# Optimization experiments

Measured on AMD Instinct MI355X. Metric: run time of the kernel, lower is better.

## Reference

```python
import jax, jax.numpy as jnp
import numpy as np

N, S, E = 8, 1024, 768
H = 12
D = E // H  # head_dim = 64
FF = 4 * E
EPS = 1e-5


def setup_inputs() -> dict:
    key = jax.random.key(0)
    ks = jax.random.split(key, 12)
    s = lambda fan_in: 1.0 / np.sqrt(fan_in)
    return {
        "x": jax.random.normal(ks[0], (N, S, E), dtype=jnp.float32),
        "ln1_g": jnp.ones((E,), jnp.float32),
        "ln1_b": jnp.zeros((E,), jnp.float32),
        "ln2_g": jnp.ones((E,), jnp.float32),
        "ln2_b": jnp.zeros((E,), jnp.float32),
        "w_attn": jax.random.normal(ks[1], (E, 3 * E), jnp.float32) * s(E),
        "b_attn": jax.random.normal(ks[2], (3 * E,), jnp.float32) * 0.02,
        "w_proj": jax.random.normal(ks[3], (E, E), jnp.float32) * s(E),
        "b_proj": jax.random.normal(ks[4], (E,), jnp.float32) * 0.02,
        "w_fc": jax.random.normal(ks[5], (E, FF), jnp.float32) * s(E),
        "b_fc": jax.random.normal(ks[6], (FF,), jnp.float32) * 0.02,
        "w_fc2": jax.random.normal(ks[7], (FF, E), jnp.float32) * s(FF),
        "b_fc2": jax.random.normal(ks[8], (E,), jnp.float32) * 0.02,
    }


def _layernorm(x, g, b):
    mu = jnp.mean(x, axis=-1, keepdims=True)
    var = jnp.var(x, axis=-1, keepdims=True)
    return (x - mu) * jax.lax.rsqrt(var + EPS) * g + b


def reference(x, ln1_g, ln1_b, ln2_g, ln2_b, w_attn, b_attn, w_proj, b_proj,
              w_fc, b_fc, w_fc2, b_fc2):
    # --- attention branch (pre-LN) ---
    h = _layernorm(x, ln1_g, ln1_b)
    qkv = h @ w_attn + b_attn                       # [N,S,3E]
    q, k, v = jnp.split(qkv, 3, axis=-1)
    q = q.reshape(N, S, H, D).transpose(0, 2, 1, 3)  # [N,H,S,D]
    k = k.reshape(N, S, H, D).transpose(0, 2, 1, 3)
    v = v.reshape(N, S, H, D).transpose(0, 2, 1, 3)
    attn = jnp.einsum('nhsd,nhtd->nhst', q, k) * (1.0 / np.sqrt(D))
    causal = jnp.tril(jnp.ones((S, S), bool))
    attn = jnp.where(causal, attn, -jnp.inf)
    p = jax.nn.softmax(attn, axis=-1)
    out = jnp.einsum('nhst,nhtd->nhsd', p, v)        # [N,H,S,D]
    out = out.transpose(0, 2, 1, 3).reshape(N, S, E)
    x = x + (out @ w_proj + b_proj)
    # --- MLP branch ---
    h2 = _layernorm(x, ln2_g, ln2_b)
    ff = jax.nn.gelu(h2 @ w_fc + b_fc, approximate=False)  # exact GELU (torch nn.GELU default)
    x = x + (ff @ w_fc2 + b_fc2)
    return x
```

## Files before the change

kernel.cpp:

```cpp
#include <hip/hip_runtime.h>
#include <hip/hip_bf16.h>
#include <stdint.h>

#define S_LEN 1024
#define E_DIM 768
#define H_N   12
#define FF_DIM 3072

typedef __hip_bfloat16 bf16;
using short8  = __attribute__((ext_vector_type(8))) short;
using short4v = __attribute__((ext_vector_type(4))) short;
using f32x4   = __attribute__((ext_vector_type(4))) float;

__device__ __forceinline__ void async_cp16(const void* g, void* l) {
  __builtin_amdgcn_global_load_lds(
      (__attribute__((address_space(1))) void*)(g),
      (__attribute__((address_space(3))) void*)(l), 16, 0, 0);
}

__global__ __launch_bounds__(256) void wcastT(const float* __restrict__ w,
                                              bf16* __restrict__ wt,
                                              int K, int N) {
  __shared__ float t[32][33];
  int bx = blockIdx.x;
  int by = blockIdx.y;
  int x = threadIdx.x & 31;
  int y = threadIdx.x >> 5;
  for (int i = y; i < 32; i += 8)
    t[i][x] = w[(size_t)(by * 32 + i) * N + bx * 32 + x];
  __syncthreads();
  for (int i = y; i < 32; i += 8)
    wt[(size_t)(bx * 32 + i) * K + by * 32 + x] = __float2bfloat16(t[x][i]);
}

__global__ __launch_bounds__(256) void ln_rows(const float* __restrict__ x,
                                               const float* __restrict__ g,
                                               const float* __restrict__ b,
                                               bf16* __restrict__ out) {
  int row = blockIdx.x;
  int tid = threadIdx.x;
  const float* xr = x + (size_t)row * E_DIM;
  float v0 = xr[tid], v1 = xr[tid + 256], v2 = xr[tid + 512];
  float s = v0 + v1 + v2;
  float ss = v0 * v0 + v1 * v1 + v2 * v2;
  for (int o = 32; o > 0; o >>= 1) {
    s  += __shfl_down(s, o);
    ss += __shfl_down(ss, o);
  }
  __shared__ float ps[4], pq[4];
  int wv = tid >> 6;
  if ((tid & 63) == 0) { ps[wv] = s; pq[wv] = ss; }
  __syncthreads();
  s  = ps[0] + ps[1] + ps[2] + ps[3];
  ss = pq[0] + pq[1] + pq[2] + pq[3];
  float mu  = s * (1.0f / E_DIM);
  float var = ss * (1.0f / E_DIM) - mu * mu;
  float rs  = rsqrtf(var + 1e-5f);
  bf16* orow = out + (size_t)row * E_DIM;
  orow[tid]       = __float2bfloat16((v0 - mu) * rs * g[tid]       + b[tid]);
  orow[tid + 256] = __float2bfloat16((v1 - mu) * rs * g[tid + 256] + b[tid + 256]);
  orow[tid + 512] = __float2bfloat16((v2 - mu) * rs * g[tid + 512] + b[tid + 512]);
}

template <int MODE>
__global__ __launch_bounds__(256) void gemm_bt(
    const bf16* __restrict__ A, const bf16* __restrict__ Bt,
    const float* __restrict__ bias, const float* __restrict__ resid,
    float* __restrict__ outf, bf16* __restrict__ ob0, bf16* __restrict__ ob1,
    bf16* __restrict__ ob2, int M, int N, int K) {
  __shared__ bf16 As[128 * 64];
  __shared__ bf16 Bs[128 * 64];
  int tid = threadIdx.x;
  int wave = tid >> 6, lane = tid & 63;
  int quad = lane >> 4, l16 = lane & 15;
  int gx = N >> 7;
  int flat = blockIdx.x;
  int y8 = flat & 7;
  int q2 = flat >> 3;
  int bx = q2 % gx;
  int by = (q2 / gx) * 8 + y8;
  int m0 = by * 128, n0 = bx * 128;
  int wm = (wave & 1) * 64, wn = (wave >> 1) * 64;
  f32x4 acc[4][4];
  for (int i = 0; i < 4; i++)
    for (int j = 0; j < 4; j++)
      for (int r = 0; r < 4; r++) acc[i][j][r] = 0.f;

  int xs = l16 & 7;

  for (int kb = 0; kb < K; kb += 64) {
    __syncthreads();
#pragma unroll
    for (int t = 0; t < 4; ++t) {
      int c = t * 256 + tid;
      int row = c >> 3;
      int cg = (((c & 7) ^ (row & 7)) << 3);
      async_cp16(A  + (size_t)(m0 + row) * K + kb + cg, &As[c * 8]);
      async_cp16(Bt + (size_t)(n0 + row) * K + kb + cg, &Bs[c * 8]);
    }
    __syncthreads();
#pragma unroll
    for (int ks = 0; ks < 2; ks++) {
      short8 af[4], bfr[4];
      for (int i = 0; i < 4; i++)
        af[i] = *(const short8*)
            &As[(wm + i * 16 + l16) * 64 + (((ks * 4 + quad) ^ xs) << 3)];
      for (int j = 0; j < 4; j++)
        bfr[j] = *(const short8*)
            &Bs[(wn + j * 16 + l16) * 64 + (((ks * 4 + quad) ^ xs) << 3)];
      for (int i = 0; i < 4; i++)
        for (int j = 0; j < 4; j++)
          acc[i][j] = __builtin_amdgcn_mfma_f32_16x16x32_bf16(bfr[j], af[i],
                                                              acc[i][j], 0, 0, 0);
    }
  }

  for (int j = 0; j < 4; j++) {
    int colb = n0 + wn + j * 16 + quad * 4;
    f32x4 b4 = *(const f32x4*)&bias[colb];
    for (int i = 0; i < 4; i++) {
      int row = m0 + wm + i * 16 + l16;
      f32x4 v = acc[i][j] + b4;
      if (MODE == 0) {
        int nn = row >> 10, s = row & 1023;
        if (colb < 768) {
          int h = colb >> 6, db = colb & 63;
          short4v pk;
          for (int r = 0; r < 4; r++)
            pk[r] = __builtin_bit_cast(short, __float2bfloat16(v[r] * 0.125f));
          *(short4v*)&ob0[(((size_t)nn * H_N + h) * S_LEN + s) * 64 + db] = pk;
        } else if (colb < 1536) {
          int c = colb - 768;
          size_t nh2 = (size_t)nn * H_N + (c >> 6);
          int d = c & 63;
          short4v pk;
          for (int r = 0; r < 4; r++)
            pk[r] = __builtin_bit_cast(short, __float2bfloat16(v[r]));
          *(short4v*)&ob1[((nh2 * 8 + (d >> 3)) * S_LEN + s) * 8 + (d & 7)] = pk;
        } else {
          int c = colb - 1536;
          size_t nh2 = (size_t)nn * H_N + (c >> 6);
          int d0 = c & 63;
          for (int r = 0; r < 4; r++)
            ob2[((nh2 * 128 + (s >> 3)) * 64 + d0 + r) * 8 + (s & 7)] =
                __float2bfloat16(v[r]);
        }
      } else if (MODE == 2) {
        short4v pk;
        for (int r = 0; r < 4; r++) {
          float x = v[r];
          float t = x * (1.59576912161f + 0.0713548162726f * x * x);
          float g = x * __builtin_amdgcn_rcpf(1.0f + __expf(-t));
          pk[r] = __builtin_bit_cast(short, __float2bfloat16(g));
        }
        *(short4v*)&ob0[(size_t)row * N + colb] = pk;
      }
    }
  }
}

__global__ __launch_bounds__(256) void gemm_bt64(
    const bf16* __restrict__ A, const bf16* __restrict__ Bt,
    const float* __restrict__ bias, const float* __restrict__ resid,
    float* __restrict__ outf, int M, int N, int K) {
  __shared__ bf16 As[128 * 64];
  __shared__ bf16 Bs[64 * 64];
  int tid = threadIdx.x;
  int wave = tid >> 6, lane = tid & 63;
  int quad = lane >> 4, l16 = lane & 15;
  int gx = N >> 6;
  int flat = blockIdx.x;
  int y8 = flat & 7;
  int q2 = flat >> 3;
  int bx = q2 % gx;
  int by = (q2 / gx) * 8 + y8;
  int m0 = by * 128, n0 = bx * 64;
  int wm = wave * 32;
  f32x4 acc[2][4];
  for (int i = 0; i < 2; i++)
    for (int j = 0; j < 4; j++)
      for (int r = 0; r < 4; r++) acc[i][j][r] = 0.f;

  int xs = l16 & 7;

  for (int kb = 0; kb < K; kb += 64) {
    __syncthreads();
#pragma unroll
    for (int t = 0; t < 4; ++t) {
      int c = t * 256 + tid;
      int row = c >> 3;
      int cg = (((c & 7) ^ (row & 7)) << 3);
      async_cp16(A + (size_t)(m0 + row) * K + kb + cg, &As[c * 8]);
    }
#pragma unroll
    for (int t = 0; t < 2; ++t) {
      int c = t * 256 + tid;
      int row = c >> 3;
      int cg = (((c & 7) ^ (row & 7)) << 3);
      async_cp16(Bt + (size_t)(n0 + row) * K + kb + cg, &Bs[c * 8]);
    }
    __syncthreads();
#pragma unroll
    for (int ks = 0; ks < 2; ks++) {
      short8 af[2], bfr[4];
      for (int i = 0; i < 2; i++)
        af[i] = *(const short8*)
            &As[(wm + i * 16 + l16) * 64 + (((ks * 4 + quad) ^ xs) << 3)];
      for (int j = 0; j < 4; j++)
        bfr[j] = *(const short8*)
            &Bs[(j * 16 + l16) * 64 + (((ks * 4 + quad) ^ xs) << 3)];
      for (int i = 0; i < 2; i++)
        for (int j = 0; j < 4; j++)
          acc[i][j] = __builtin_amdgcn_mfma_f32_16x16x32_bf16(bfr[j], af[i],
                                                              acc[i][j], 0, 0, 0);
    }
  }

  for (int j = 0; j < 4; j++) {
    int colb = n0 + j * 16 + quad * 4;
    f32x4 b4 = *(const f32x4*)&bias[colb];
    for (int i = 0; i < 2; i++) {
      int row = m0 + wm + i * 16 + l16;
      size_t idx = (size_t)row * N + colb;
      f32x4 rv = *(const f32x4*)&resid[idx];
      *(f32x4*)&outf[idx] = acc[i][j] + b4 + rv;
    }
  }
}

__global__ __launch_bounds__(256) void attn_fwd(
    const bf16* __restrict__ q, const bf16* __restrict__ kg,
    const bf16* __restrict__ vg, bf16* __restrict__ out) {
  __shared__ bf16 kt2[8 * 64 * 8];
  __shared__ bf16 vt2[8 * 64 * 8];
  __shared__ bf16 pba[4][16 * 68];
  __shared__ bf16 pbb[4][16 * 68];
  int flat = blockIdx.x;
  int xcd = flat & 7;
  int j = flat >> 3;
  int a = j & 7;
  int g = j >> 3;
  int nh = xcd * 12 + g;
  int b = 15 - a;
  int n = nh / H_N, h = nh % H_N;
  int tid = threadIdx.x, wave = tid >> 6, lane = tid & 63;
  int quad = lane >> 4, l16 = lane & 15;
  const bf16* qp = q  + (size_t)nh * S_LEN * 64;
  const bf16* kp = kg + (size_t)nh * 8 * S_LEN * 8;
  const bf16* vp = vg + (size_t)nh * 128 * 64 * 8;
  int qra = a * 64 + wave * 16;
  int qrb = b * 64 + wave * 16;

  short8 qfa[2], qfb[2];
  qfa[0] = *(const short8*)&qp[(size_t)(qra + l16) * 64 + quad * 8];
  qfa[1] = *(const short8*)&qp[(size_t)(qra + l16) * 64 + 32 + quad * 8];
  qfb[0] = *(const short8*)&qp[(size_t)(qrb + l16) * 64 + quad * 8];
  qfb[1] = *(const short8*)&qp[(size_t)(qrb + l16) * 64 + 32 + quad * 8];

  f32x4 oaa[4], oab[4];
  for (int dt = 0; dt < 4; dt++)
    for (int r = 0; r < 4; r++) { oaa[dt][r] = 0.f; oab[dt][r] = 0.f; }
  float lia = 0.f, lib = 0.f;

  for (int kb = 0; kb <= b; ++kb) {
    bool act_a = (kb <= a);
    __syncthreads();
    for (int t = 0; t < 2; ++t) {
      int s = t * 256 + tid;
      int c = s >> 6, e = s & 63;
      async_cp16(kp + ((size_t)c * S_LEN + kb * 64 + e) * 8, &kt2[(size_t)s * 8]);
      async_cp16(vp + ((size_t)(kb * 8 + c) * 64 + e) * 8, &vt2[(size_t)s * 8]);
    }
    __syncthreads();

    f32x4 sb4[4], sa4[4];
    for (int nt = 0; nt < 4; nt++) {
      for (int r = 0; r < 4; r++) { sb4[nt][r] = -10.f; sa4[nt][r] = -10.f; }
      for (int ks = 0; ks < 2; ks++) {
        short8 kf = *(const short8*)
            &kt2[(size_t)((ks * 4 + quad) * 64 + nt * 16 + l16) * 8];
        sb4[nt] = __builtin_amdgcn_mfma_f32_16x16x32_bf16(kf, qfb[ks], sb4[nt], 0, 0, 0);
        if (act_a)
          sa4[nt] = __builtin_amdgcn_mfma_f32_16x16x32_bf16(kf, qfa[ks], sa4[nt], 0, 0, 0);
      }
    }
    if (kb == b) {
      int ql = wave * 16 + l16;
      for (int nt = 0; nt < 4; nt++)
        for (int r = 0; r < 4; r++)
          if (nt * 16 + quad * 4 + r > ql) sb4[nt][r] = -INFINITY;
    }
    if (kb == a) {
      int ql = wave * 16 + l16;
      for (int nt = 0; nt < 4; nt++)
        for (int r = 0; r < 4; r++)
          if (nt * 16 + quad * 4 + r > ql) sa4[nt][r] = -INFINITY;
    }

    float rsb = 0.f;
    for (int nt = 0; nt < 4; nt++)
      for (int r = 0; r < 4; r++) {
        float p = __expf(sb4[nt][r]);
        sb4[nt][r] = p;
        rsb += p;
      }
    rsb += __shfl_xor(rsb, 16);
    rsb += __shfl_xor(rsb, 32);
    lib += rsb;
    bf16* pwb = pbb[wave];
    for (int nt = 0; nt < 4; nt++) {
      short4v pk;
      for (int r = 0; r < 4; r++)
        pk[r] = __builtin_bit_cast(short, __float2bfloat16(sb4[nt][r]));
      *(short4v*)&pwb[l16 * 68 + nt * 16 + quad * 4] = pk;
    }
    if (act_a) {
      float rsa = 0.f;
      for (int nt = 0; nt < 4; nt++)
        for (int r = 0; r < 4; r++) {
          float p = __expf(sa4[nt][r]);
          sa4[nt][r] = p;
          rsa += p;
        }
      rsa += __shfl_xor(rsa, 16);
      rsa += __shfl_xor(rsa, 32);
      lia += rsa;
      bf16* pwa = pba[wave];
      for (int nt = 0; nt < 4; nt++) {
        short4v pk;
        for (int r = 0; r < 4; r++)
          pk[r] = __builtin_bit_cast(short, __float2bfloat16(sa4[nt][r]));
        *(short4v*)&pwa[l16 * 68 + nt * 16 + quad * 4] = pk;
      }
    }
    asm volatile("s_waitcnt lgkmcnt(0)" ::: "memory");

    for (int ks = 0; ks < 2; ks++) {
      short8 pfb = *(const short8*)&pbb[wave][l16 * 68 + ks * 32 + quad * 8];
      short8 pfa;
      if (act_a) pfa = *(const short8*)&pba[wave][l16 * 68 + ks * 32 + quad * 8];
      for (int dt = 0; dt < 4; dt++) {
        short8 vf = *(const short8*)
            &vt2[(size_t)((ks * 4 + quad) * 64 + dt * 16 + l16) * 8];
        oab[dt] = __builtin_amdgcn_mfma_f32_16x16x32_bf16(vf, pfb, oab[dt], 0, 0, 0);
        if (act_a)
          oaa[dt] = __builtin_amdgcn_mfma_f32_16x16x32_bf16(vf, pfa, oaa[dt], 0, 0, 0);
      }
    }
  }

  float inva = 1.0f / lia, invb = 1.0f / lib;
  int ta = n * S_LEN + qra + l16;
  int tb = n * S_LEN + qrb + l16;
  for (int dt = 0; dt < 4; dt++) {
    short4v ova, ovb;
    for (int r = 0; r < 4; r++) {
      ova[r] = __builtin_bit_cast(short, __float2bfloat16(oaa[dt][r] * inva));
      ovb[r] = __builtin_bit_cast(short, __float2bfloat16(oab[dt][r] * invb));
    }
    *(short4v*)&out[(size_t)ta * E_DIM + h * 64 + dt * 16 + quad * 4] = ova;
    *(short4v*)&out[(size_t)tb * E_DIM + h * 64 + dt * 16 + quad * 4] = ovb;
  }
}

extern "C" void kernel_launch(void* const* d_in, const int* in_sizes, int n_in,
                              void* d_out, int out_size, void* d_ws, size_t ws_size,
                              hipStream_t stream) {
  (void)in_sizes; (void)n_in; (void)out_size; (void)ws_size;
  const float* x      = (const float*)d_in[0];
  const float* ln1_g  = (const float*)d_in[1];
  const float* ln1_b  = (const float*)d_in[2];
  const float* ln2_g  = (const float*)d_in[3];
  const float* ln2_b  = (const float*)d_in[4];
  const float* w_attn = (const float*)d_in[5];
  const float* b_attn = (const float*)d_in[6];
  const float* w_proj = (const float*)d_in[7];
  const float* b_proj = (const float*)d_in[8];
  const float* w_fc   = (const float*)d_in[9];
  const float* b_fc   = (const float*)d_in[10];
  const float* w_fc2  = (const float*)d_in[11];
  const float* b_fc2  = (const float*)d_in[12];
  float* out = (float*)d_out;

  char* ws = (char*)d_ws;
  bf16* wt_attn = (bf16*)(ws);
  bf16* wt_proj = (bf16*)(ws + 3538944);
  bf16* wt_fc   = (bf16*)(ws + 4718592);
  bf16* wt_fc2  = (bf16*)(ws + 9437184);
  bf16* hbuf    = (bf16*)(ws + 14155776);
  float* x2     = (float*)(ws + 26738688);
  bf16* qb      = (bf16*)(ws + 51904512);
  bf16* kbuf    = (bf16*)(ws + 64487424);
  bf16* vtb     = (bf16*)(ws + 77070336);
  bf16* ao      = (bf16*)(ws + 89653248);
  bf16* ff      = qb;

  dim3 blk(256);
  wcastT<<<dim3(2304 / 32, 768 / 32), blk, 0, stream>>>(w_attn, wt_attn, 768, 2304);
  wcastT<<<dim3(768 / 32, 768 / 32), blk, 0, stream>>>(w_proj, wt_proj, 768, 768);
  wcastT<<<dim3(3072 / 32, 768 / 32), blk, 0, stream>>>(w_fc, wt_fc, 768, 3072);
  wcastT<<<dim3(768 / 32, 3072 / 32), blk, 0, stream>>>(w_fc2, wt_fc2, 3072, 768);

  ln_rows<<<8192, blk, 0, stream>>>(x, ln1_g, ln1_b, hbuf);

  gemm_bt<0><<<dim3(18 * 64), blk, 0, stream>>>(
      hbuf, wt_attn, b_attn, nullptr, nullptr, qb, kbuf, vtb, 8192, 2304, 768);

  attn_fwd<<<dim3(768), blk, 0, stream>>>(qb, kbuf, vtb, ao);

  gemm_bt64<<<dim3(12 * 64), blk, 0, stream>>>(
      ao, wt_proj, b_proj, x, x2, 8192, 768, 768);

  ln_rows<<<8192, blk, 0, stream>>>(x2, ln2_g, ln2_b, hbuf);

  gemm_bt<2><<<dim3(24 * 64), blk, 0, stream>>>(
      hbuf, wt_fc, b_fc, nullptr, nullptr, ff, nullptr, nullptr, 8192, 3072, 768);

  gemm_bt64<<<dim3(12 * 64), blk, 0, stream>>>(
      ff, wt_fc2, b_fc2, x2, out, 8192, 768, 3072);
}
```

Measured before the change: 360.8 us.

## Double-buffer LDS tiles in GEMM and attention kernels to overlap loads

Adds ping-pong LDS buffers to both GEMM kernels and the attention kernel, so the next K/V or A/B tile is fetched asynchronously while the current tile is multiplied. Each iteration first copies the current tile's fragments into registers, then issues the prefetch, and uses one barrier per iteration instead of two. The goal is to hide global-load latency behind the MFMA work. In exchange it doubles LDS use (64KB for the 128x128 GEMM) and raises register pressure, which can lower occupancy.

```diff
diff --git a/kernel.cpp b/kernel.cpp
--- a/kernel.cpp
+++ b/kernel.cpp
@@ -68,8 +68,8 @@
     const float* __restrict__ bias, const float* __restrict__ resid,
     float* __restrict__ outf, bf16* __restrict__ ob0, bf16* __restrict__ ob1,
     bf16* __restrict__ ob2, int M, int N, int K) {
-  __shared__ bf16 As[128 * 64];
-  __shared__ bf16 Bs[128 * 64];
+  __shared__ bf16 As[2][128 * 64];
+  __shared__ bf16 Bs[2][128 * 64];
   int tid = threadIdx.x;
   int wave = tid >> 6, lane = tid & 63;
   int quad = lane >> 4, l16 = lane & 15;
@@ -87,32 +87,49 @@
       for (int r = 0; r < 4; r++) acc[i][j][r] = 0.f;
 
   int xs = l16 & 7;
-
-  for (int kb = 0; kb < K; kb += 64) {
+  int srow = tid >> 3;
+  int cg = (((tid & 7) ^ (srow & 7)) << 3);
+  const bf16* aptr = A  + (size_t)(m0 + srow) * K + cg;
+  const bf16* bptr = Bt + (size_t)(n0 + srow) * K + cg;
+
+  int nkb = K >> 6;
+  {
+    bf16* la = &As[0][0] + tid * 8;
+    bf16* lb = &Bs[0][0] + tid * 8;
+#pragma unroll
+    for (int t = 0; t < 4; ++t) {
+      async_cp16(aptr + (size_t)t * 32 * K, la + t * 2048);
+      async_cp16(bptr + (size_t)t * 32 * K, lb + t * 2048);
+    }
+  }
+  for (int ik = 0; ik < nkb; ++ik) {
+    int cur = ik & 1;
     __syncthreads();
-#pragma unroll
-    for (int t = 0; t < 4; ++t) {
-      int c = t * 256 + tid;
-      int row = c >> 3;
-      int cg = (((c & 7) ^ (row & 7)) << 3);
-      async_cp16(A  + (size_t)(m0 + row) * K + kb + cg, &As[c * 8]);
-      async_cp16(Bt + (size_t)(n0 + row) * K + kb + cg, &Bs[c * 8]);
-    }
-    __syncthreads();
+    short8 af[2][4], bfr[2][4];
 #pragma unroll
     for (int ks = 0; ks < 2; ks++) {
-      short8 af[4], bfr[4];
+      int ko = (((ks * 4 + quad) ^ xs) << 3);
       for (int i = 0; i < 4; i++)
-        af[i] = *(const short8*)
-            &As[(wm + i * 16 + l16) * 64 + (((ks * 4 + quad) ^ xs) << 3)];
+        af[ks][i] = *(const short8*)&As[cur][(wm + i * 16 + l16) * 64 + ko];
       for (int j = 0; j < 4; j++)
-        bfr[j] = *(const short8*)
-            &Bs[(wn + j * 16 + l16) * 64 + (((ks * 4 + quad) ^ xs) << 3)];
+        bfr[ks][j] = *(const short8*)&Bs[cur][(wn + j * 16 + l16) * 64 + ko];
+    }
+    if (ik + 1 < nkb) {
+      size_t ko = (size_t)(ik + 1) * 64;
+      bf16* la = &As[cur ^ 1][0] + tid * 8;
+      bf16* lb = &Bs[cur ^ 1][0] + tid * 8;
+#pragma unroll
+      for (int t = 0; t < 4; ++t) {
+        async_cp16(aptr + ko + (size_t)t * 32 * K, la + t * 2048);
+        async_cp16(bptr + ko + (size_t)t * 32 * K, lb + t * 2048);
+      }
+    }
+#pragma unroll
+    for (int ks = 0; ks < 2; ks++)
       for (int i = 0; i < 4; i++)
         for (int j = 0; j < 4; j++)
-          acc[i][j] = __builtin_amdgcn_mfma_f32_16x16x32_bf16(bfr[j], af[i],
-                                                              acc[i][j], 0, 0, 0);
-    }
+          acc[i][j] = __builtin_amdgcn_mfma_f32_16x16x32_bf16(
+              bfr[ks][j], af[ks][i], acc[i][j], 0, 0, 0);
   }
 
   for (int j = 0; j < 4; j++) {
@@ -163,8 +180,8 @@
     const bf16* __restrict__ A, const bf16* __restrict__ Bt,
     const float* __restrict__ bias, const float* __restrict__ resid,
     float* __restrict__ outf, int M, int N, int K) {
-  __shared__ bf16 As[128 * 64];
-  __shared__ bf16 Bs[64 * 64];
+  __shared__ bf16 As[2][128 * 64];
+  __shared__ bf16 Bs[2][64 * 64];
   int tid = threadIdx.x;
   int wave = tid >> 6, lane = tid & 63;
   int quad = lane >> 4, l16 = lane & 15;
@@ -182,38 +199,51 @@
       for (int r = 0; r < 4; r++) acc[i][j][r] = 0.f;
 
   int xs = l16 & 7;
-
-  for (int kb = 0; kb < K; kb += 64) {
+  int srow = tid >> 3;
+  int cg = (((tid & 7) ^ (srow & 7)) << 3);
+  const bf16* aptr = A  + (size_t)(m0 + srow) * K + cg;
+  const bf16* bptr = Bt + (size_t)(n0 + srow) * K + cg;
+
+  int nkb = K >> 6;
+  {
+    bf16* la = &As[0][0] + tid * 8;
+    bf16* lb = &Bs[0][0] + tid * 8;
+#pragma unroll
+    for (int t = 0; t < 4; ++t)
+      async_cp16(aptr + (size_t)t * 32 * K, la + t * 2048);
+#pragma unroll
+    for (int t = 0; t < 2; ++t)
+      async_cp16(bptr + (size_t)t * 32 * K, lb + t * 2048);
+  }
+  for (int ik = 0; ik < nkb; ++ik) {
+    int cur = ik & 1;
     __syncthreads();
-#pragma unroll
-    for (int t = 0; t < 4; ++t) {
-      int c = t * 256 + tid;
-      int row = c >> 3;
-      int cg = (((c & 7) ^ (row & 7)) << 3);
-      async_cp16(A + (size_t)(m0 + row) * K + kb + cg, &As[c * 8]);
-    }
-#pragma unroll
-    for (int t = 0; t < 2; ++t) {
-      int c = t * 256 + tid;
-      int row = c >> 3;
-      int cg = (((c & 7) ^ (row & 7)) << 3);
-      async_cp16(Bt + (size_t)(n0 + row) * K + kb + cg, &Bs[c * 8]);
-    }
-    __syncthreads();
+    short8 af[2][2], bfr[2][4];
 #pragma unroll
     for (int ks = 0; ks < 2; ks++) {
-      short8 af[2], bfr[4];
+      int ko = (((ks * 4 + quad) ^ xs) << 3);
       for (int i = 0; i < 2; i++)
-        af[i] = *(const short8*)
-            &As[(wm + i * 16 + l16) * 64 + (((ks * 4 + quad) ^ xs) << 3)];
+        af[ks][i] = *(const short8*)&As[cur][(wm + i * 16 + l16) * 64 + ko];
       for (int j = 0; j < 4; j++)
-        bfr[j] = *(const short8*)
-            &Bs[(j * 16 + l16) * 64 + (((ks * 4 + quad) ^ xs) << 3)];
+        bfr[ks][j] = *(const short8*)&Bs[cur][(j * 16 + l16) * 64 + ko];
+    }
+    if (ik + 1 < nkb) {
+      size_t ko = (size_t)(ik + 1) * 64;
+      bf16* la = &As[cur ^ 1][0] + tid * 8;
+      bf16* lb = &Bs[cur ^ 1][0] + tid * 8;
+#pragma unroll
+      for (int t = 0; t < 4; ++t)
+        async_cp16(aptr + ko + (size_t)t * 32 * K, la + t * 2048);
+#pragma unroll
+      for (int t = 0; t < 2; ++t)
+        async_cp16(bptr + ko + (size_t)t * 32 * K, lb + t * 2048);
+    }
+#pragma unroll
+    for (int ks = 0; ks < 2; ks++)
       for (int i = 0; i < 2; i++)
         for (int j = 0; j < 4; j++)
-          acc[i][j] = __builtin_amdgcn_mfma_f32_16x16x32_bf16(bfr[j], af[i],
-                                                              acc[i][j], 0, 0, 0);
-    }
+          acc[i][j] = __builtin_amdgcn_mfma_f32_16x16x32_bf16(
+              bfr[ks][j], af[ks][i], acc[i][j], 0, 0, 0);
   }
 
   for (int j = 0; j < 4; j++) {
@@ -231,8 +261,8 @@
 __global__ __launch_bounds__(256) void attn_fwd(
     const bf16* __restrict__ q, const bf16* __restrict__ kg,
     const bf16* __restrict__ vg, bf16* __restrict__ out) {
-  __shared__ bf16 kt2[8 * 64 * 8];
-  __shared__ bf16 vt2[8 * 64 * 8];
+  __shared__ bf16 kt2[2][8 * 64 * 8];
+  __shared__ bf16 vt2[2][8 * 64 * 8];
   __shared__ bf16 pba[4][16 * 68];
   __shared__ bf16 pbb[4][16 * 68];
   int flat = blockIdx.x;
@@ -257,31 +287,59 @@
   qfb[0] = *(const short8*)&qp[(size_t)(qrb + l16) * 64 + quad * 8];
   qfb[1] = *(const short8*)&qp[(size_t)(qrb + l16) * 64 + 32 + quad * 8];
 
+  const bf16* kbase = kp + (((size_t)(tid >> 6) * S_LEN) + (tid & 63)) * 8;
+  const bf16* vbase = vp + (((size_t)(tid >> 6) * 64) + (tid & 63)) * 8;
+
   f32x4 oaa[4], oab[4];
   for (int dt = 0; dt < 4; dt++)
     for (int r = 0; r < 4; r++) { oaa[dt][r] = 0.f; oab[dt][r] = 0.f; }
   float lia = 0.f, lib = 0.f;
 
+  {
+    bf16* lk = &kt2[0][0] + tid * 8;
+    bf16* lv = &vt2[0][0] + tid * 8;
+#pragma unroll
+    for (int t = 0; t < 2; ++t) {
+      async_cp16(kbase + (size_t)t * 4 * S_LEN * 8, lk + t * 2048);
+      async_cp16(vbase + (size_t)t * 2048, lv + t * 2048);
+    }
+  }
+
   for (int kb = 0; kb <= b; ++kb) {
     bool act_a = (kb <= a);
+    int cur = kb & 1;
     __syncthreads();
-    for (int t = 0; t < 2; ++t) {
-      int s = t * 256 + tid;
-      int c = s >> 6, e = s & 63;
-      async_cp16(kp + ((size_t)c * S_LEN + kb * 64 + e) * 8, &kt2[(size_t)s * 8]);
-      async_cp16(vp + ((size_t)(kb * 8 + c) * 64 + e) * 8, &vt2[(size_t)s * 8]);
-    }
-    __syncthreads();
+
+    short8 kf[2][4], vf[2][4];
+#pragma unroll
+    for (int ks = 0; ks < 2; ks++)
+      for (int nt = 0; nt < 4; nt++) {
+        kf[ks][nt] = *(const short8*)
+            &kt2[cur][(size_t)((ks * 4 + quad) * 64 + nt * 16 + l16) * 8];
+        vf[ks][nt] = *(const short8*)
+            &vt2[cur][(size_t)((ks * 4 + quad) * 64 + nt * 16 + l16) * 8];
+      }
+    if (kb < b) {
+      bf16* lk = &kt2[cur ^ 1][0] + tid * 8;
+      bf16* lv = &vt2[cur ^ 1][0] + tid * 8;
+      size_t kko = (size_t)(kb + 1) * 512;
+      size_t vko = (size_t)(kb + 1) * 4096;
+#pragma unroll
+      for (int t = 0; t < 2; ++t) {
+        async_cp16(kbase + kko + (size_t)t * 4 * S_LEN * 8, lk + t * 2048);
+        async_cp16(vbase + vko + (size_t)t * 2048, lv + t * 2048);
+      }
+    }
 
     f32x4 sb4[4], sa4[4];
     for (int nt = 0; nt < 4; nt++) {
       for (int r = 0; r < 4; r++) { sb4[nt][r] = -10.f; sa4[nt][r] = -10.f; }
       for (int ks = 0; ks < 2; ks++) {
-        short8 kf = *(const short8*)
-            &kt2[(size_t)((ks * 4 + quad) * 64 + nt * 16 + l16) * 8];
-        sb4[nt] = __builtin_amdgcn_mfma_f32_16x16x32_bf16(kf, qfb[ks], sb4[nt], 0, 0, 0);
+        sb4[nt] = __builtin_amdgcn_mfma_f32_16x16x32_bf16(kf[ks][nt], qfb[ks],
+                                                          sb4[nt], 0, 0, 0);
         if (act_a)
-          sa4[nt] = __builtin_amdgcn_mfma_f32_16x16x32_bf16(kf, qfa[ks], sa4[nt], 0, 0, 0);
+          sa4[nt] = __builtin_amdgcn_mfma_f32_16x16x32_bf16(kf[ks][nt], qfa[ks],
+                                                            sa4[nt], 0, 0, 0);
       }
     }
     if (kb == b) {
@@ -340,11 +398,11 @@
       short8 pfa;
       if (act_a) pfa = *(const short8*)&pba[wave][l16 * 68 + ks * 32 + quad * 8];
       for (int dt = 0; dt < 4; dt++) {
-        short8 vf = *(const short8*)
-            &vt2[(size_t)((ks * 4 + quad) * 64 + dt * 16 + l16) * 8];
-        oab[dt] = __builtin_amdgcn_mfma_f32_16x16x32_bf16(vf, pfb, oab[dt], 0, 0, 0);
+        oab[dt] = __builtin_amdgcn_mfma_f32_16x16x32_bf16(vf[ks][dt], pfb,
+                                                          oab[dt], 0, 0, 0);
         if (act_a)
-          oaa[dt] = __builtin_amdgcn_mfma_f32_16x16x32_bf16(vf, pfa, oaa[dt], 0, 0, 0);
+          oaa[dt] = __builtin_amdgcn_mfma_f32_16x16x32_bf16(vf[ks][dt], pfa,
+                                                            oaa[dt], 0, 0, 0);
       }
     }
   }
```

Result: no change. 367.9 us (+2.0%).
